# Kernel optimization log

Measured on AMD Instinct MI355X. Metric: run time of the kernel, lower is better.

Reference implementation:

```python
import jax, jax.numpy as jnp
import numpy as np

N_EMBED = 1024
N_HEADS = 16
HEAD_SIZE = N_EMBED // N_HEADS
B, T = 4, 2048
LN_EPS = 1e-5


def _layer_norm(x, gamma, beta):
    mu = jnp.mean(x, axis=-1, keepdims=True)
    var = jnp.var(x, axis=-1, keepdims=True)
    return (x - mu) * jax.lax.rsqrt(var + LN_EPS) * gamma + beta


def setup_inputs() -> dict:
    key = jax.random.key(0)
    ks = jax.random.split(key, 12)
    s = 1.0 / np.sqrt(N_EMBED)
    sh = 1.0 / np.sqrt(4 * N_EMBED)
    return {
        "x": jax.random.normal(ks[0], (B, T, N_EMBED), jnp.float32),
        "Wk": jax.random.uniform(ks[1], (N_EMBED, N_EMBED), jnp.float32, -s, s),
        "Wq": jax.random.uniform(ks[2], (N_EMBED, N_EMBED), jnp.float32, -s, s),
        "Wv": jax.random.uniform(ks[3], (N_EMBED, N_EMBED), jnp.float32, -s, s),
        "Wproj": jax.random.uniform(ks[4], (N_EMBED, N_EMBED), jnp.float32, -s, s),
        "bproj": jax.random.uniform(ks[5], (N_EMBED,), jnp.float32, -s, s),
        "W1": jax.random.uniform(ks[6], (N_EMBED, 4 * N_EMBED), jnp.float32, -s, s),
        "b1": jax.random.uniform(ks[7], (4 * N_EMBED,), jnp.float32, -s, s),
        "W2": jax.random.uniform(ks[8], (4 * N_EMBED, N_EMBED), jnp.float32, -sh, sh),
        "b2": jax.random.uniform(ks[9], (N_EMBED,), jnp.float32, -sh, sh),
        "g1": jnp.ones((N_EMBED,), jnp.float32),
        "beta1": jnp.zeros((N_EMBED,), jnp.float32),
        "g2": jnp.ones((N_EMBED,), jnp.float32),
        "beta2": jnp.zeros((N_EMBED,), jnp.float32),
    }


def reference(x, Wk, Wq, Wv, Wproj, bproj, W1, b1, W2, b2, g1, beta1, g2, beta2):
    Bt, Tt, C = x.shape
    h = _layer_norm(x, g1, beta1)
    # project and split heads: (B, H, T, D)
    def heads(W):
        return (h @ W).reshape(Bt, Tt, N_HEADS, HEAD_SIZE).transpose(0, 2, 1, 3)
    q, k, v = heads(Wq), heads(Wk), heads(Wv)
    wei = jnp.einsum("bhtd,bhsd->bhts", q, k) / np.sqrt(HEAD_SIZE)
    causal = jnp.tril(jnp.ones((Tt, Tt), bool))
    wei = jnp.where(causal, wei, -jnp.inf)
    wei = jax.nn.softmax(wei, axis=-1)
    out = jnp.einsum("bhts,bhsd->bhtd", wei, v)
    out = out.transpose(0, 2, 1, 3).reshape(Bt, Tt, C)
    x = x + out @ Wproj + bproj
    h2 = _layer_norm(x, g2, beta2)
    ff = jax.nn.relu(h2 @ W1 + b1) @ W2 + b2
    return x + ff
```

## Files before the change

### kernel.cpp

```cpp
#include <hip/hip_runtime.h>
#include <stdint.h>

typedef __bf16 bf16x8 __attribute__((ext_vector_type(8)));
typedef float f32x4 __attribute__((ext_vector_type(4)));
typedef unsigned short u16x8 __attribute__((ext_vector_type(8)));
typedef unsigned short u16x4 __attribute__((ext_vector_type(4)));
typedef unsigned int u32x2 __attribute__((ext_vector_type(2)));
typedef float fvec4 __attribute__((ext_vector_type(4)));

__device__ __forceinline__ unsigned short f2b(float f) {
  unsigned u = __builtin_bit_cast(unsigned, f);
  return (unsigned short)((u + 0x7fffu + ((u >> 16) & 1u)) >> 16);
}

__device__ __forceinline__ bf16x8 ldfrag(const unsigned short* p) {
  return __builtin_bit_cast(bf16x8, *(const u16x8*)p);
}

__device__ __forceinline__ float fexp2(float x) {
  float r;
  asm("v_exp_f32 %0, %1" : "=v"(r) : "v"(x));
  return r;
}

__device__ __forceinline__ unsigned cvtpk(float a, float b) {
  unsigned r;
  asm("v_cvt_pk_bf16_f32 %0, %1, %2" : "=v"(r) : "v"(a), "v"(b));
  return r;
}

__device__ __forceinline__ void gload_lds16(const void* g, void* l) {
  auto gp = reinterpret_cast<const __attribute__((address_space(1))) void*>(
      reinterpret_cast<uintptr_t>(g));
  auto lp = reinterpret_cast<__attribute__((address_space(3))) void*>(
      reinterpret_cast<uintptr_t>(l));
  __builtin_amdgcn_global_load_lds(gp, lp, 16, 0, 0);
}

__global__ void transpose_cast(const float* __restrict__ W, unsigned short* __restrict__ Wt,
                               int K, int N) {
  __shared__ float tile[32][33];
  const int n0 = blockIdx.x * 32, k0 = blockIdx.y * 32;
  const int tx = threadIdx.x, ty = threadIdx.y;
#pragma unroll
  for (int j = 0; j < 4; ++j)
    tile[ty + j * 8][tx] = W[(size_t)(k0 + ty + j * 8) * N + n0 + tx];
  __syncthreads();
#pragma unroll
  for (int j = 0; j < 4; ++j)
    Wt[(size_t)(n0 + ty + j * 8) * K + k0 + tx] = f2b(tile[tx][ty + j * 8]);
}

__global__ void ln_kernel(const float* __restrict__ X, const float* __restrict__ g,
                          const float* __restrict__ be, unsigned short* __restrict__ H) {
  const int row = (blockIdx.x * blockDim.x + threadIdx.x) >> 6;
  const int l = threadIdx.x & 63;
  const float* xr = X + (size_t)row * 1024;
  fvec4 v[4];
  float s = 0.f, sq = 0.f;
#pragma unroll
  for (int i = 0; i < 4; ++i) {
    v[i] = *(const fvec4*)(xr + i * 256 + l * 4);
#pragma unroll
    for (int j = 0; j < 4; ++j) { s += v[i][j]; sq += v[i][j] * v[i][j]; }
  }
#pragma unroll
  for (int off = 32; off >= 1; off >>= 1) {
    s += __shfl_xor(s, off);
    sq += __shfl_xor(sq, off);
  }
  const float mean = s * (1.f / 1024.f);
  const float var = sq * (1.f / 1024.f) - mean * mean;
  const float rstd = rsqrtf(var + 1e-5f);
#pragma unroll
  for (int i = 0; i < 4; ++i) {
    const int col = i * 256 + l * 4;
    fvec4 gg = *(const fvec4*)(g + col);
    fvec4 bb = *(const fvec4*)(be + col);
    u16x4 o;
#pragma unroll
    for (int j = 0; j < 4; ++j) o[j] = f2b((v[i][j] - mean) * rstd * gg[j] + bb[j]);
    *(u16x4*)(H + (size_t)row * 1024 + col) = o;
  }
}

template <int BM, int EPI>
__global__ __launch_bounds__(512, 1) void gemmS(
    const unsigned short* __restrict__ A, const unsigned short* __restrict__ Bt,
    const float* __restrict__ bias, const float* __restrict__ resid,
    float* __restrict__ Cf, unsigned short* __restrict__ Cb,
    unsigned short* __restrict__ pK, unsigned short* __restrict__ pVT,
    int N, int K, int ntiles) {
  constexpr int ASZ = BM * 64;
  constexpr int BSZ = 16384;
  constexpr int BUFSZ = ASZ + BSZ;
  constexpr int UA = ASZ / 8192;
  constexpr int UNITS = UA + 2;
  constexpr int MF = BM / 32;
  __shared__ __align__(16) char lds[4 * BUFSZ];

  const int tid = threadIdx.x;
  const int w = tid >> 6, l = tid & 63;
  const int wr = w >> 2, wc = w & 3;
  const int kg = l >> 4, fr = l & 15;
  const int xtiles = N / 256;
  const int nblk = (int)gridDim.x;

  int Aoff[MF], Boff[4];
#pragma unroll
  for (int m = 0; m < MF; ++m) {
    const int r = wr * (BM / 2) + m * 16 + fr;
    Aoff[m] = r * 64 + ((kg ^ ((r >> 1) & 3)) << 4);
  }
#pragma unroll
  for (int n = 0; n < 4; ++n) {
    const int rn = wc * 64 + n * 16 + fr;
    Boff[n] = ASZ + rn * 64 + ((kg ^ ((rn >> 1) & 3)) << 4);
  }

  for (int tl = (int)blockIdx.x; tl < ntiles; tl += nblk) {
    if (tl != (int)blockIdx.x) __builtin_amdgcn_s_barrier();
    const int q8 = ntiles >> 3;
    const int swz = (tl & 7) * q8 + (tl >> 3);
    const size_t am0 = (size_t)(swz / xtiles) * BM;
    const size_t bn0 = (size_t)(swz % xtiles) * 256;

    const char* src[UNITS];
#pragma unroll
    for (int u = 0; u < UA; ++u) {
      const int flat = u * 512 + tid;
      const int row = flat >> 2;
      const int scb = ((flat & 3) << 4) ^ (((row >> 1) & 3) << 4);
      src[u] = (const char*)(A + (am0 + row) * K) + scb;
    }
#pragma unroll
    for (int u = 0; u < 2; ++u) {
      const int flat = u * 512 + tid;
      const int row = flat >> 2;
      const int scb = ((flat & 3) << 4) ^ (((row >> 1) & 3) << 4);
      src[UA + u] = (const char*)(Bt + (bn0 + row) * K) + scb;
    }

    f32x4 acc[MF][4];
#pragma unroll
    for (int m = 0; m < MF; ++m)
#pragma unroll
      for (int n = 0; n < 4; ++n) acc[m][n] = (f32x4){0.f, 0.f, 0.f, 0.f};

    auto stage = [&](int sb) {
#pragma unroll
      for (int u = 0; u < UNITS; ++u) {
        gload_lds16(src[u], lds + sb * BUFSZ + u * 8192 + tid * 16);
        src[u] += 64;
      }
    };

    const int NT = K >> 5;
    stage(0);
    stage(1);
    asm volatile("s_waitcnt vmcnt(%0)" ::"i"(UNITS) : "memory");
    __builtin_amdgcn_s_barrier();

    int cb0 = 0, sb = 2;
    for (int kt = 0; kt < NT; ++kt) {
      if (kt + 2 < NT) stage(sb);
      bf16x8 af[MF], bf[4];
#pragma unroll
      for (int m = 0; m < MF; ++m)
        af[m] = ldfrag((const unsigned short*)(lds + cb0 + Aoff[m]));
#pragma unroll
      for (int n = 0; n < 4; ++n)
        bf[n] = ldfrag((const unsigned short*)(lds + cb0 + Boff[n]));
      __builtin_amdgcn_s_setprio(1);
#pragma unroll
      for (int m = 0; m < MF; ++m)
#pragma unroll
        for (int n = 0; n < 4; ++n)
          acc[m][n] = __builtin_amdgcn_mfma_f32_16x16x32_bf16(af[m], bf[n], acc[m][n], 0, 0, 0);
      __builtin_amdgcn_s_setprio(0);
      if (kt + 2 < NT) {
        asm volatile("s_waitcnt vmcnt(%0)" ::"i"(UNITS) : "memory");
        __builtin_amdgcn_s_barrier();
      } else if (kt + 1 < NT) {
        asm volatile("s_waitcnt vmcnt(0)" ::: "memory");
        __builtin_amdgcn_s_barrier();
      }
      cb0 += BUFSZ;
      if (cb0 == 4 * BUFSZ) cb0 = 0;
      sb += 1;
      if (sb == 4) sb = 0;
    }

#pragma unroll
    for (int m = 0; m < MF; ++m) {
      const size_t row0 = am0 + wr * (BM / 2) + m * 16 + kg * 4;
#pragma unroll
      for (int n = 0; n < 4; ++n) {
        const size_t col = bn0 + wc * 64 + n * 16 + fr;
        if (EPI == 3) {
          if (bn0 < 1024) {
#pragma unroll
            for (int r = 0; r < 4; ++r) Cb[(row0 + r) * 1024 + col] = f2b(acc[m][n][r]);
          } else if (bn0 < 2048) {
#pragma unroll
            for (int r = 0; r < 4; ++r) pK[(row0 + r) * 1024 + col - 1024] = f2b(acc[m][n][r]);
          } else {
            const int c2 = (int)col - 2048;
            const int hh = c2 >> 6, dd = c2 & 63;
            const int bb = (int)(row0 >> 11), tt = (int)(row0 & 2047);
            u16x4 pv;
#pragma unroll
            for (int r = 0; r < 4; ++r) pv[r] = f2b(acc[m][n][r]);
            *(u16x4*)(pVT + (((size_t)bb * 16 + hh) * 64 + dd) * 2048 + tt) = pv;
          }
        } else {
          const float bv = (EPI >= 1) ? bias[col] : 0.f;
#pragma unroll
          for (int r = 0; r < 4; ++r) {
            const size_t idx = (row0 + r) * N + col;
            float v = acc[m][n][r] + bv;
            if (EPI == 1) v = fmaxf(v, 0.f);
            if (EPI == 2) {
              Cf[idx] = v + resid[idx];
            } else {
              Cb[idx] = f2b(v);
            }
          }
        }
      }
    }
  }
}

#define PSTR 72
#define SC2 0.18033688f
__global__ __launch_bounds__(256, 2) void attn_kernel(const unsigned short* __restrict__ Qb,
                                                      const unsigned short* __restrict__ Kb,
                                                      const unsigned short* __restrict__ VT,
                                                      unsigned short* __restrict__ ATT) {
  __shared__ __align__(16) char ldsK[3 * 8192];
  __shared__ __align__(16) unsigned short Pl[4][64 * PSTR];
  const int tid = threadIdx.x;
  const int w = tid >> 6, l = tid & 63;
  const int kg = l >> 4, fr = l & 15;
  const int bh = blockIdx.x;
  const int b = bh >> 4, h = bh & 15;
  const int yy = (int)blockIdx.y;
  const int qt = (yy < 4) ? 7 - yy : yy - 4;
  const int q0 = qt * 256 + w * 64;
  const size_t rbase = (size_t)b * 2048;
  const unsigned short* vtb = VT + (size_t)bh * 64 * 2048;
  const f32x4 fz = {0.f, 0.f, 0.f, 0.f};

  const int rowoff = tid >> 3;
  const int cbsw = ((tid & 7) * 16) ^ ((rowoff & 7) << 4);
  const char* ksrc = (const char*)(Kb + rbase * 1024 + h * 64) + (size_t)rowoff * 2048 + cbsw;

  int koff[4][2];
#pragma unroll
  for (int sg = 0; sg < 4; ++sg)
#pragma unroll
    for (int c = 0; c < 2; ++c)
      koff[sg][c] = (sg * 16 + fr) * 128 + ((c * 64 + kg * 16) ^ ((fr & 7) << 4));

  bf16x8 bq[4][2];
#pragma unroll
  for (int qg = 0; qg < 4; ++qg) {
    const unsigned short* qrow = Qb + (rbase + q0 + qg * 16 + fr) * 1024 + h * 64;
#pragma unroll
    for (int c = 0; c < 2; ++c) bq[qg][c] = ldfrag(qrow + c * 32 + kg * 8);
  }

  f32x4 o[4][4];
#pragma unroll
  for (int qg = 0; qg < 4; ++qg)
#pragma unroll
    for (int nd = 0; nd < 4; ++nd) o[qg][nd] = (f32x4){0.f, 0.f, 0.f, 0.f};
  float m_run2[4] = {-1e30f, -1e30f, -1e30f, -1e30f};
  float l_run[4] = {0.f, 0.f, 0.f, 0.f};

  auto stage = [&](int t, int sbuf) {
    gload_lds16(ksrc + (size_t)(t * 64) * 2048, ldsK + sbuf * 8192 + tid * 16);
    gload_lds16(ksrc + (size_t)(t * 64 + 32) * 2048, ldsK + sbuf * 8192 + 4096 + tid * 16);
  };

  auto softmax_qg = [&](int qg, int s0, f32x4 (&stq)[4]) -> float {
    const int qa = q0 + qg * 16 + fr;
    float vals[16];
    if (s0 + 63 <= q0 + qg * 16) {
#pragma unroll
      for (int sg = 0; sg < 4; ++sg)
#pragma unroll
        for (int r = 0; r < 4; ++r) vals[sg * 4 + r] = stq[sg][r];
    } else {
#pragma unroll
      for (int sg = 0; sg < 4; ++sg)
#pragma unroll
        for (int r = 0; r < 4; ++r) {
          const int sa = s0 + sg * 16 + kg * 4 + r;
          vals[sg * 4 + r] = (sa > qa) ? -1e30f : stq[sg][r];
        }
    }
    float m5[5];
#pragma unroll
    for (int i = 0; i < 5; ++i)
      m5[i] = fmaxf(fmaxf(vals[3 * i], vals[3 * i + 1]), vals[3 * i + 2]);
    const float vmax =
        fmaxf(fmaxf(fmaxf(m5[0], m5[1]), m5[2]), fmaxf(fmaxf(m5[3], m5[4]), vals[15]));
    const float tm2 = vmax * SC2;
    if (__any(tm2 > m_run2[qg] + 8.f)) {
      float tmax2 = tm2;
      tmax2 = fmaxf(tmax2, __shfl_xor(tmax2, 16));
      tmax2 = fmaxf(tmax2, __shfl_xor(tmax2, 32));
      const float m_new2 = fmaxf(m_run2[qg], tmax2);
      const float alpha = fexp2(m_run2[qg] - m_new2);
      m_run2[qg] = m_new2;
      l_run[qg] *= alpha;
      float al[4];
#pragma unroll
      for (int r = 0; r < 4; ++r) al[r] = __shfl(alpha, kg * 4 + r);
#pragma unroll
      for (int nd = 0; nd < 4; ++nd)
#pragma unroll
        for (int r = 0; r < 4; ++r) o[qg][nd][r] *= al[r];
    }
    const float nm2 = -m_run2[qg];
    float psum = 0.f;
    unsigned pk[8];
#pragma unroll
    for (int i = 0; i < 8; ++i) {
      const float p0 = fexp2(__builtin_fmaf(vals[2 * i], SC2, nm2));
      const float p1 = fexp2(__builtin_fmaf(vals[2 * i + 1], SC2, nm2));
      psum += p0 + p1;
      pk[i] = cvtpk(p0, p1);
    }
#pragma unroll
    for (int sg = 0; sg < 4; ++sg) {
      u32x2 w2 = {pk[2 * sg], pk[2 * sg + 1]};
      *(u32x2*)(&Pl[w][(qg * 16 + fr) * PSTR + sg * 16 + kg * 4]) = w2;
    }
    return psum;
  };

  auto compute = [&](int s0, int cbb) {
    if (s0 > q0 + 63) return;
    bf16x8 vb[4][2];
#pragma unroll
    for (int nd = 0; nd < 4; ++nd)
#pragma unroll
      for (int ks = 0; ks < 2; ++ks)
        vb[nd][ks] = ldfrag(vtb + (size_t)(nd * 16 + fr) * 2048 + s0 + ks * 32 + kg * 8);

    float psv[4];
#pragma unroll
    for (int qp = 0; qp < 2; ++qp) {
      f32x4 st[4][2];
#pragma unroll
      for (int sg = 0; sg < 4; ++sg) {
        const bf16x8 ka0 = ldfrag((const unsigned short*)(ldsK + cbb + koff[sg][0]));
        const bf16x8 ka1 = ldfrag((const unsigned short*)(ldsK + cbb + koff[sg][1]));
#pragma unroll
        for (int qh = 0; qh < 2; ++qh)
          st[sg][qh] = __builtin_amdgcn_mfma_f32_16x16x32_bf16(
              ka1, bq[qp * 2 + qh][1],
              __builtin_amdgcn_mfma_f32_16x16x32_bf16(ka0, bq[qp * 2 + qh][0], fz, 0, 0, 0),
              0, 0, 0);
      }
#pragma unroll
      for (int qh = 0; qh < 2; ++qh) {
        f32x4 stq[4];
#pragma unroll
        for (int sg = 0; sg < 4; ++sg) stq[sg] = st[sg][qh];
        psv[qp * 2 + qh] = softmax_qg(qp * 2 + qh, s0, stq);
      }
    }

    {
      float a[4], c[4];
#pragma unroll
      for (int qg = 0; qg < 4; ++qg) a[qg] = __shfl_xor(psv[qg], 16);
#pragma unroll
      for (int qg = 0; qg < 4; ++qg) psv[qg] += a[qg];
#pragma unroll
      for (int qg = 0; qg < 4; ++qg) c[qg] = __shfl_xor(psv[qg], 32);
#pragma unroll
      for (int qg = 0; qg < 4; ++qg) l_run[qg] += psv[qg] + c[qg];
    }

#pragma unroll
    for (int qg = 0; qg < 4; ++qg)
#pragma unroll
      for (int ks = 0; ks < 2; ++ks) {
        const bf16x8 pa = ldfrag(&Pl[w][(qg * 16 + fr) * PSTR + ks * 32 + kg * 8]);
#pragma unroll
        for (int nd = 0; nd < 4; ++nd)
          o[qg][nd] = __builtin_amdgcn_mfma_f32_16x16x32_bf16(pa, vb[nd][ks], o[qg][nd], 0, 0, 0);
      }
  };

  const int NT = 4 * qt + 4;
  stage(0, 0);
  stage(1, 1);
  asm volatile("s_waitcnt vmcnt(2)" ::: "memory");
  __builtin_amdgcn_s_barrier();
  int cb = 0, sb = 2;
  for (int t = 0; t < NT; ++t) {
    if (t + 2 < NT) stage(t + 2, sb);
    compute(t * 64, cb * 8192);
    if (t + 2 < NT) {
      asm volatile("s_waitcnt vmcnt(2)" ::: "memory");
      __builtin_amdgcn_s_barrier();
    } else if (t + 1 < NT) {
      asm volatile("s_waitcnt vmcnt(0)" ::: "memory");
      __builtin_amdgcn_s_barrier();
    }
    cb += 1; if (cb == 3) cb = 0;
    sb += 1; if (sb == 3) sb = 0;
  }

#pragma unroll
  for (int qg = 0; qg < 4; ++qg) {
    const float li = __builtin_amdgcn_rcpf(l_run[qg]);
    float linv[4];
#pragma unroll
    for (int r = 0; r < 4; ++r) linv[r] = __shfl(li, kg * 4 + r);
#pragma unroll
    for (int nd = 0; nd < 4; ++nd)
#pragma unroll
      for (int r = 0; r < 4; ++r) {
        const size_t row = rbase + q0 + qg * 16 + kg * 4 + r;
        ATT[row * 1024 + h * 64 + nd * 16 + fr] = f2b(o[qg][nd][r] * linv[r]);
      }
  }
}

extern "C" void kernel_launch(void* const* d_in, const int* in_sizes, int n_in, void* d_out,
                              int out_size, void* d_ws, size_t ws_size, hipStream_t stream) {
  const float* x = (const float*)d_in[0];
  const float* Wk = (const float*)d_in[1];
  const float* Wq = (const float*)d_in[2];
  const float* Wv = (const float*)d_in[3];
  const float* Wproj = (const float*)d_in[4];
  const float* bproj = (const float*)d_in[5];
  const float* W1 = (const float*)d_in[6];
  const float* b1 = (const float*)d_in[7];
  const float* W2 = (const float*)d_in[8];
  const float* b2 = (const float*)d_in[9];
  const float* g1 = (const float*)d_in[10];
  const float* beta1 = (const float*)d_in[11];
  const float* g2 = (const float*)d_in[12];
  const float* beta2 = (const float*)d_in[13];
  float* out = (float*)d_out;
  unsigned short* wsu = (unsigned short*)d_ws;

  const size_t o_qkvW = 0;
  const size_t o_projW = o_qkvW + 3072 * 1024;
  const size_t o_W1 = o_projW + 1024 * 1024;
  const size_t o_W2 = o_W1 + 4096 * 1024;
  const size_t o_H = o_W2 + 1024 * 4096;
  const size_t o_Q = o_H + (size_t)8192 * 1024;
  const size_t o_K = o_Q + (size_t)8192 * 1024;
  const size_t o_VT = o_K + (size_t)8192 * 1024;
  const size_t o_ATT = o_VT + (size_t)8192 * 1024;
  const size_t o_FF1 = o_Q;

  dim3 tpb(32, 8);
  transpose_cast<<<dim3(32, 32), tpb, 0, stream>>>(Wq, wsu + o_qkvW, 1024, 1024);
  transpose_cast<<<dim3(32, 32), tpb, 0, stream>>>(Wk, wsu + o_qkvW + 1024 * 1024, 1024, 1024);
  transpose_cast<<<dim3(32, 32), tpb, 0, stream>>>(Wv, wsu + o_qkvW + 2 * 1024 * 1024, 1024, 1024);
  transpose_cast<<<dim3(32, 32), tpb, 0, stream>>>(Wproj, wsu + o_projW, 1024, 1024);
  transpose_cast<<<dim3(128, 32), tpb, 0, stream>>>(W1, wsu + o_W1, 1024, 4096);
  transpose_cast<<<dim3(32, 128), tpb, 0, stream>>>(W2, wsu + o_W2, 4096, 1024);

  ln_kernel<<<2048, 256, 0, stream>>>(x, g1, beta1, wsu + o_H);

  gemmS<128, 3><<<256, 512, 0, stream>>>(wsu + o_H, wsu + o_qkvW, nullptr, nullptr, nullptr,
                                         wsu + o_Q, wsu + o_K, wsu + o_VT, 3072, 1024, 768);

  attn_kernel<<<dim3(64, 8), 256, 0, stream>>>(wsu + o_Q, wsu + o_K, wsu + o_VT, wsu + o_ATT);

  gemmS<128, 2><<<256, 512, 0, stream>>>(wsu + o_ATT, wsu + o_projW, bproj, x, out, nullptr,
                                         nullptr, nullptr, 1024, 1024, 256);

  ln_kernel<<<2048, 256, 0, stream>>>(out, g2, beta2, wsu + o_H);

  gemmS<256, 1><<<256, 512, 0, stream>>>(wsu + o_H, wsu + o_W1, b1, nullptr, nullptr,
                                         wsu + o_FF1, nullptr, nullptr, 4096, 1024, 512);

  gemmS<128, 2><<<256, 512, 0, stream>>>(wsu + o_FF1, wsu + o_W2, b2, out, out, nullptr,
                                         nullptr, nullptr, 1024, 4096, 256);
}
```

Baseline: 342.9 us.

## Pair causal query tiles per block for balanced attention work

```diff
diff --git a/kernel.cpp b/kernel.cpp
--- a/kernel.cpp
+++ b/kernel.cpp
@@ -239,15 +239,13 @@
                                                       const unsigned short* __restrict__ VT,
                                                       unsigned short* __restrict__ ATT) {
   __shared__ __align__(16) char ldsK[3 * 8192];
-  __shared__ __align__(16) unsigned short Pl[4][64 * PSTR];
+  __shared__ __align__(16) unsigned short Pl[4][32 * PSTR];
   const int tid = threadIdx.x;
   const int w = tid >> 6, l = tid & 63;
   const int kg = l >> 4, fr = l & 15;
   const int bh = blockIdx.x;
   const int b = bh >> 4, h = bh & 15;
   const int yy = (int)blockIdx.y;
-  const int qt = (yy < 4) ? 7 - yy : yy - 4;
-  const int q0 = qt * 256 + w * 64;
   const size_t rbase = (size_t)b * 2048;
   const unsigned short* vtb = VT + (size_t)bh * 64 * 2048;
   const f32x4 fz = {0.f, 0.f, 0.f, 0.f};
@@ -262,175 +260,170 @@
 #pragma unroll
     for (int c = 0; c < 2; ++c)
       koff[sg][c] = (sg * 16 + fr) * 128 + ((c * 64 + kg * 16) ^ ((fr & 7) << 4));
-
-  bf16x8 bq[4][2];
-#pragma unroll
-  for (int qg = 0; qg < 4; ++qg) {
-    const unsigned short* qrow = Qb + (rbase + q0 + qg * 16 + fr) * 1024 + h * 64;
-#pragma unroll
-    for (int c = 0; c < 2; ++c) bq[qg][c] = ldfrag(qrow + c * 32 + kg * 8);
-  }
-
-  f32x4 o[4][4];
-#pragma unroll
-  for (int qg = 0; qg < 4; ++qg)
-#pragma unroll
-    for (int nd = 0; nd < 4; ++nd) o[qg][nd] = (f32x4){0.f, 0.f, 0.f, 0.f};
-  float m_run2[4] = {-1e30f, -1e30f, -1e30f, -1e30f};
-  float l_run[4] = {0.f, 0.f, 0.f, 0.f};
 
   auto stage = [&](int t, int sbuf) {
     gload_lds16(ksrc + (size_t)(t * 64) * 2048, ldsK + sbuf * 8192 + tid * 16);
     gload_lds16(ksrc + (size_t)(t * 64 + 32) * 2048, ldsK + sbuf * 8192 + 4096 + tid * 16);
   };
 
-  auto softmax_qg = [&](int qg, int s0, f32x4 (&stq)[4]) -> float {
-    const int qa = q0 + qg * 16 + fr;
-    float vals[16];
-    if (s0 + 63 <= q0 + qg * 16) {
-#pragma unroll
-      for (int sg = 0; sg < 4; ++sg)
-#pragma unroll
-        for (int r = 0; r < 4; ++r) vals[sg * 4 + r] = stq[sg][r];
-    } else {
-#pragma unroll
-      for (int sg = 0; sg < 4; ++sg)
-#pragma unroll
-        for (int r = 0; r < 4; ++r) {
-          const int sa = s0 + sg * 16 + kg * 4 + r;
-          vals[sg * 4 + r] = (sa > qa) ? -1e30f : stq[sg][r];
-        }
-    }
-    float m5[5];
-#pragma unroll
-    for (int i = 0; i < 5; ++i)
-      m5[i] = fmaxf(fmaxf(vals[3 * i], vals[3 * i + 1]), vals[3 * i + 2]);
-    const float vmax =
-        fmaxf(fmaxf(fmaxf(m5[0], m5[1]), m5[2]), fmaxf(fmaxf(m5[3], m5[4]), vals[15]));
-    const float tm2 = vmax * SC2;
-    if (__any(tm2 > m_run2[qg] + 8.f)) {
-      float tmax2 = tm2;
-      tmax2 = fmaxf(tmax2, __shfl_xor(tmax2, 16));
-      tmax2 = fmaxf(tmax2, __shfl_xor(tmax2, 32));
-      const float m_new2 = fmaxf(m_run2[qg], tmax2);
-      const float alpha = fexp2(m_run2[qg] - m_new2);
-      m_run2[qg] = m_new2;
-      l_run[qg] *= alpha;
-      float al[4];
-#pragma unroll
-      for (int r = 0; r < 4; ++r) al[r] = __shfl(alpha, kg * 4 + r);
+  for (int pass = 0; pass < 2; ++pass) {
+    const int qt = pass ? yy : 15 - yy;
+    const int q0 = qt * 128 + w * 32;
+
+    bf16x8 bq[2][2];
+#pragma unroll
+    for (int qg = 0; qg < 2; ++qg) {
+      const unsigned short* qrow = Qb + (rbase + q0 + qg * 16 + fr) * 1024 + h * 64;
+#pragma unroll
+      for (int c = 0; c < 2; ++c) bq[qg][c] = ldfrag(qrow + c * 32 + kg * 8);
+    }
+
+    f32x4 o[2][4];
+#pragma unroll
+    for (int qg = 0; qg < 2; ++qg)
+#pragma unroll
+      for (int nd = 0; nd < 4; ++nd) o[qg][nd] = (f32x4){0.f, 0.f, 0.f, 0.f};
+    float m_run2[2] = {-1e30f, -1e30f}, l_run[2] = {0.f, 0.f};
+
+    auto compute = [&](int s0, int cbb) {
+      if (s0 > q0 + 31) return;
+      bf16x8 vb[4][2];
 #pragma unroll
       for (int nd = 0; nd < 4; ++nd)
 #pragma unroll
-        for (int r = 0; r < 4; ++r) o[qg][nd][r] *= al[r];
-    }
-    const float nm2 = -m_run2[qg];
-    float psum = 0.f;
-    unsigned pk[8];
-#pragma unroll
-    for (int i = 0; i < 8; ++i) {
-      const float p0 = fexp2(__builtin_fmaf(vals[2 * i], SC2, nm2));
-      const float p1 = fexp2(__builtin_fmaf(vals[2 * i + 1], SC2, nm2));
-      psum += p0 + p1;
-      pk[i] = cvtpk(p0, p1);
-    }
-#pragma unroll
-    for (int sg = 0; sg < 4; ++sg) {
-      u32x2 w2 = {pk[2 * sg], pk[2 * sg + 1]};
-      *(u32x2*)(&Pl[w][(qg * 16 + fr) * PSTR + sg * 16 + kg * 4]) = w2;
-    }
-    return psum;
-  };
-
-  auto compute = [&](int s0, int cbb) {
-    if (s0 > q0 + 63) return;
-    bf16x8 vb[4][2];
-#pragma unroll
-    for (int nd = 0; nd < 4; ++nd)
-#pragma unroll
-      for (int ks = 0; ks < 2; ++ks)
-        vb[nd][ks] = ldfrag(vtb + (size_t)(nd * 16 + fr) * 2048 + s0 + ks * 32 + kg * 8);
-
-    float psv[4];
-#pragma unroll
-    for (int qp = 0; qp < 2; ++qp) {
+        for (int ks = 0; ks < 2; ++ks)
+          vb[nd][ks] = ldfrag(vtb + (size_t)(nd * 16 + fr) * 2048 + s0 + ks * 32 + kg * 8);
+
       f32x4 st[4][2];
 #pragma unroll
       for (int sg = 0; sg < 4; ++sg) {
         const bf16x8 ka0 = ldfrag((const unsigned short*)(ldsK + cbb + koff[sg][0]));
         const bf16x8 ka1 = ldfrag((const unsigned short*)(ldsK + cbb + koff[sg][1]));
 #pragma unroll
-        for (int qh = 0; qh < 2; ++qh)
-          st[sg][qh] = __builtin_amdgcn_mfma_f32_16x16x32_bf16(
-              ka1, bq[qp * 2 + qh][1],
-              __builtin_amdgcn_mfma_f32_16x16x32_bf16(ka0, bq[qp * 2 + qh][0], fz, 0, 0, 0),
-              0, 0, 0);
-      }
-#pragma unroll
-      for (int qh = 0; qh < 2; ++qh) {
-        f32x4 stq[4];
-#pragma unroll
-        for (int sg = 0; sg < 4; ++sg) stq[sg] = st[sg][qh];
-        psv[qp * 2 + qh] = softmax_qg(qp * 2 + qh, s0, stq);
-      }
-    }
-
-    {
-      float a[4], c[4];
-#pragma unroll
-      for (int qg = 0; qg < 4; ++qg) a[qg] = __shfl_xor(psv[qg], 16);
-#pragma unroll
-      for (int qg = 0; qg < 4; ++qg) psv[qg] += a[qg];
-#pragma unroll
-      for (int qg = 0; qg < 4; ++qg) c[qg] = __shfl_xor(psv[qg], 32);
-#pragma unroll
-      for (int qg = 0; qg < 4; ++qg) l_run[qg] += psv[qg] + c[qg];
-    }
-
-#pragma unroll
-    for (int qg = 0; qg < 4; ++qg)
-#pragma unroll
-      for (int ks = 0; ks < 2; ++ks) {
-        const bf16x8 pa = ldfrag(&Pl[w][(qg * 16 + fr) * PSTR + ks * 32 + kg * 8]);
-#pragma unroll
-        for (int nd = 0; nd < 4; ++nd)
-          o[qg][nd] = __builtin_amdgcn_mfma_f32_16x16x32_bf16(pa, vb[nd][ks], o[qg][nd], 0, 0, 0);
-      }
-  };
-
-  const int NT = 4 * qt + 4;
-  stage(0, 0);
-  stage(1, 1);
-  asm volatile("s_waitcnt vmcnt(2)" ::: "memory");
-  __builtin_amdgcn_s_barrier();
-  int cb = 0, sb = 2;
-  for (int t = 0; t < NT; ++t) {
-    if (t + 2 < NT) stage(t + 2, sb);
-    compute(t * 64, cb * 8192);
-    if (t + 2 < NT) {
-      asm volatile("s_waitcnt vmcnt(2)" ::: "memory");
-      __builtin_amdgcn_s_barrier();
-    } else if (t + 1 < NT) {
-      asm volatile("s_waitcnt vmcnt(0)" ::: "memory");
-      __builtin_amdgcn_s_barrier();
-    }
-    cb += 1; if (cb == 3) cb = 0;
-    sb += 1; if (sb == 3) sb = 0;
-  }
-
-#pragma unroll
-  for (int qg = 0; qg < 4; ++qg) {
-    const float li = __builtin_amdgcn_rcpf(l_run[qg]);
-    float linv[4];
-#pragma unroll
-    for (int r = 0; r < 4; ++r) linv[r] = __shfl(li, kg * 4 + r);
-#pragma unroll
-    for (int nd = 0; nd < 4; ++nd)
-#pragma unroll
-      for (int r = 0; r < 4; ++r) {
-        const size_t row = rbase + q0 + qg * 16 + kg * 4 + r;
-        ATT[row * 1024 + h * 64 + nd * 16 + fr] = f2b(o[qg][nd][r] * linv[r]);
-      }
+        for (int qg = 0; qg < 2; ++qg)
+          st[sg][qg] = __builtin_amdgcn_mfma_f32_16x16x32_bf16(
+              ka1, bq[qg][1],
+              __builtin_amdgcn_mfma_f32_16x16x32_bf16(ka0, bq[qg][0], fz, 0, 0, 0), 0, 0, 0);
+      }
+
+      float psv[2];
+#pragma unroll
+      for (int qg = 0; qg < 2; ++qg) {
+        const int qa = q0 + qg * 16 + fr;
+        float vals[16];
+        if (s0 + 63 <= q0 + qg * 16) {
+#pragma unroll
+          for (int sg = 0; sg < 4; ++sg)
+#pragma unroll
+            for (int r = 0; r < 4; ++r) vals[sg * 4 + r] = st[sg][qg][r];
+        } else {
+#pragma unroll
+          for (int sg = 0; sg < 4; ++sg)
+#pragma unroll
+            for (int r = 0; r < 4; ++r) {
+              const int sa = s0 + sg * 16 + kg * 4 + r;
+              vals[sg * 4 + r] = (sa > qa) ? -1e30f : st[sg][qg][r];
+            }
+        }
+        float m5[5];
+#pragma unroll
+        for (int i = 0; i < 5; ++i)
+          m5[i] = fmaxf(fmaxf(vals[3 * i], vals[3 * i + 1]), vals[3 * i + 2]);
+        const float vmax =
+            fmaxf(fmaxf(fmaxf(m5[0], m5[1]), m5[2]), fmaxf(fmaxf(m5[3], m5[4]), vals[15]));
+        const float tm2 = vmax * SC2;
+        if (__any(tm2 > m_run2[qg] + 8.f)) {
+          float tmax2 = tm2;
+          tmax2 = fmaxf(tmax2, __shfl_xor(tmax2, 16));
+          tmax2 = fmaxf(tmax2, __shfl_xor(tmax2, 32));
+          const float m_new2 = fmaxf(m_run2[qg], tmax2);
+          const float alpha = fexp2(m_run2[qg] - m_new2);
+          m_run2[qg] = m_new2;
+          l_run[qg] *= alpha;
+          float al[4];
+#pragma unroll
+          for (int r = 0; r < 4; ++r) al[r] = __shfl(alpha, kg * 4 + r);
+#pragma unroll
+          for (int nd = 0; nd < 4; ++nd)
+#pragma unroll
+            for (int r = 0; r < 4; ++r) o[qg][nd][r] *= al[r];
+        }
+        const float nm2 = -m_run2[qg];
+        float psum = 0.f;
+        unsigned pk[8];
+#pragma unroll
+        for (int i = 0; i < 8; ++i) {
+          const float p0 = fexp2(__builtin_fmaf(vals[2 * i], SC2, nm2));
+          const float p1 = fexp2(__builtin_fmaf(vals[2 * i + 1], SC2, nm2));
+          psum += p0 + p1;
+          pk[i] = cvtpk(p0, p1);
+        }
+        psv[qg] = psum;
+#pragma unroll
+        for (int sg = 0; sg < 4; ++sg) {
+          u32x2 w2 = {pk[2 * sg], pk[2 * sg + 1]};
+          *(u32x2*)(&Pl[w][(qg * 16 + fr) * PSTR + sg * 16 + kg * 4]) = w2;
+        }
+      }
+
+      {
+        const float a0 = __shfl_xor(psv[0], 16);
+        const float a1 = __shfl_xor(psv[1], 16);
+        psv[0] += a0;
+        psv[1] += a1;
+        const float b0 = __shfl_xor(psv[0], 32);
+        const float b1 = __shfl_xor(psv[1], 32);
+        l_run[0] += psv[0] + b0;
+        l_run[1] += psv[1] + b1;
+      }
+
+#pragma unroll
+      for (int qg = 0; qg < 2; ++qg)
+#pragma unroll
+        for (int ks = 0; ks < 2; ++ks) {
+          const bf16x8 pa = ldfrag(&Pl[w][(qg * 16 + fr) * PSTR + ks * 32 + kg * 8]);
+#pragma unroll
+          for (int nd = 0; nd < 4; ++nd)
+            o[qg][nd] =
+                __builtin_amdgcn_mfma_f32_16x16x32_bf16(pa, vb[nd][ks], o[qg][nd], 0, 0, 0);
+        }
+    };
+
+    const int NT = 2 * qt + 2;
+    if (pass) __builtin_amdgcn_s_barrier();
+    stage(0, 0);
+    stage(1, 1);
+    asm volatile("s_waitcnt vmcnt(2)" ::: "memory");
+    __builtin_amdgcn_s_barrier();
+    int cb = 0, sb = 2;
+    for (int t = 0; t < NT; ++t) {
+      if (t + 2 < NT) stage(t + 2, sb);
+      compute(t * 64, cb * 8192);
+      if (t + 2 < NT) {
+        asm volatile("s_waitcnt vmcnt(2)" ::: "memory");
+        __builtin_amdgcn_s_barrier();
+      } else if (t + 1 < NT) {
+        asm volatile("s_waitcnt vmcnt(0)" ::: "memory");
+        __builtin_amdgcn_s_barrier();
+      }
+      cb += 1; if (cb == 3) cb = 0;
+      sb += 1; if (sb == 3) sb = 0;
+    }
+
+#pragma unroll
+    for (int qg = 0; qg < 2; ++qg) {
+      const float li = __builtin_amdgcn_rcpf(l_run[qg]);
+      float linv[4];
+#pragma unroll
+      for (int r = 0; r < 4; ++r) linv[r] = __shfl(li, kg * 4 + r);
+#pragma unroll
+      for (int nd = 0; nd < 4; ++nd)
+#pragma unroll
+        for (int r = 0; r < 4; ++r) {
+          const size_t row = rbase + q0 + qg * 16 + kg * 4 + r;
+          ATT[row * 1024 + h * 64 + nd * 16 + fr] = f2b(o[qg][nd][r] * linv[r]);
+        }
+    }
   }
 }
 
```

Measured after the change: 349.1 us. Within noise of the previous version (+1.8%).

## Deepen GEMM K-tile to 64 with triple buffering and fixed 128-row M tile

Applied to the files above, without the earlier changes.

```diff
diff --git a/kernel.cpp b/kernel.cpp
--- a/kernel.cpp
+++ b/kernel.cpp
@@ -84,20 +84,17 @@
   }
 }
 
-template <int BM, int EPI>
+template <int EPI>
 __global__ __launch_bounds__(512, 1) void gemmS(
     const unsigned short* __restrict__ A, const unsigned short* __restrict__ Bt,
     const float* __restrict__ bias, const float* __restrict__ resid,
     float* __restrict__ Cf, unsigned short* __restrict__ Cb,
     unsigned short* __restrict__ pK, unsigned short* __restrict__ pVT,
     int N, int K, int ntiles) {
-  constexpr int ASZ = BM * 64;
-  constexpr int BSZ = 16384;
+  constexpr int ASZ = 16384;
+  constexpr int BSZ = 32768;
   constexpr int BUFSZ = ASZ + BSZ;
-  constexpr int UA = ASZ / 8192;
-  constexpr int UNITS = UA + 2;
-  constexpr int MF = BM / 32;
-  __shared__ __align__(16) char lds[4 * BUFSZ];
+  __shared__ __align__(16) char lds[3 * BUFSZ];
 
   const int tid = threadIdx.x;
   const int w = tid >> 6, l = tid & 63;
@@ -106,94 +103,104 @@
   const int xtiles = N / 256;
   const int nblk = (int)gridDim.x;
 
-  int Aoff[MF], Boff[4];
-#pragma unroll
-  for (int m = 0; m < MF; ++m) {
-    const int r = wr * (BM / 2) + m * 16 + fr;
-    Aoff[m] = r * 64 + ((kg ^ ((r >> 1) & 3)) << 4);
-  }
-#pragma unroll
-  for (int n = 0; n < 4; ++n) {
-    const int rn = wc * 64 + n * 16 + fr;
-    Boff[n] = ASZ + rn * 64 + ((kg ^ ((rn >> 1) & 3)) << 4);
+  int Aoff[2][4], Boff[2][4];
+#pragma unroll
+  for (int kk = 0; kk < 2; ++kk) {
+#pragma unroll
+    for (int m = 0; m < 4; ++m) {
+      const int r = wr * 64 + m * 16 + fr;
+      Aoff[kk][m] = r * 128 + (((kk * 4 + kg) ^ (r & 7)) << 4);
+    }
+#pragma unroll
+    for (int n = 0; n < 4; ++n) {
+      const int rn = wc * 64 + n * 16 + fr;
+      Boff[kk][n] = ASZ + rn * 128 + (((kk * 4 + kg) ^ (rn & 7)) << 4);
+    }
   }
 
   for (int tl = (int)blockIdx.x; tl < ntiles; tl += nblk) {
     if (tl != (int)blockIdx.x) __builtin_amdgcn_s_barrier();
     const int q8 = ntiles >> 3;
     const int swz = (tl & 7) * q8 + (tl >> 3);
-    const size_t am0 = (size_t)(swz / xtiles) * BM;
+    const size_t am0 = (size_t)(swz / xtiles) * 128;
     const size_t bn0 = (size_t)(swz % xtiles) * 256;
 
-    const char* src[UNITS];
-#pragma unroll
-    for (int u = 0; u < UA; ++u) {
-      const int flat = u * 512 + tid;
-      const int row = flat >> 2;
-      const int scb = ((flat & 3) << 4) ^ (((row >> 1) & 3) << 4);
-      src[u] = (const char*)(A + (am0 + row) * K) + scb;
-    }
+    const char* src[6];
 #pragma unroll
     for (int u = 0; u < 2; ++u) {
       const int flat = u * 512 + tid;
-      const int row = flat >> 2;
-      const int scb = ((flat & 3) << 4) ^ (((row >> 1) & 3) << 4);
-      src[UA + u] = (const char*)(Bt + (bn0 + row) * K) + scb;
-    }
-
-    f32x4 acc[MF][4];
-#pragma unroll
-    for (int m = 0; m < MF; ++m)
+      const int row = flat >> 3, c = flat & 7;
+      src[u] = (const char*)(A + (am0 + row) * K) + ((c ^ (row & 7)) << 4);
+    }
+#pragma unroll
+    for (int u = 0; u < 4; ++u) {
+      const int flat = u * 512 + tid;
+      const int row = flat >> 3, c = flat & 7;
+      src[2 + u] = (const char*)(Bt + (bn0 + row) * K) + ((c ^ (row & 7)) << 4);
+    }
+
+    f32x4 acc[4][4];
+#pragma unroll
+    for (int m = 0; m < 4; ++m)
 #pragma unroll
       for (int n = 0; n < 4; ++n) acc[m][n] = (f32x4){0.f, 0.f, 0.f, 0.f};
 
     auto stage = [&](int sb) {
-#pragma unroll
-      for (int u = 0; u < UNITS; ++u) {
-        gload_lds16(src[u], lds + sb * BUFSZ + u * 8192 + tid * 16);
-        src[u] += 64;
+      char* Ld = lds + sb * BUFSZ;
+#pragma unroll
+      for (int u = 0; u < 2; ++u) {
+        gload_lds16(src[u], Ld + u * 8192 + tid * 16);
+        src[u] += 128;
+      }
+#pragma unroll
+      for (int u = 0; u < 4; ++u) {
+        gload_lds16(src[2 + u], Ld + ASZ + u * 8192 + tid * 16);
+        src[2 + u] += 128;
       }
     };
 
-    const int NT = K >> 5;
+    const int NT = K >> 6;
     stage(0);
     stage(1);
-    asm volatile("s_waitcnt vmcnt(%0)" ::"i"(UNITS) : "memory");
+    asm volatile("s_waitcnt vmcnt(6)" ::: "memory");
     __builtin_amdgcn_s_barrier();
 
     int cb0 = 0, sb = 2;
     for (int kt = 0; kt < NT; ++kt) {
       if (kt + 2 < NT) stage(sb);
-      bf16x8 af[MF], bf[4];
-#pragma unroll
-      for (int m = 0; m < MF; ++m)
-        af[m] = ldfrag((const unsigned short*)(lds + cb0 + Aoff[m]));
-#pragma unroll
-      for (int n = 0; n < 4; ++n)
-        bf[n] = ldfrag((const unsigned short*)(lds + cb0 + Boff[n]));
-      __builtin_amdgcn_s_setprio(1);
-#pragma unroll
-      for (int m = 0; m < MF; ++m)
+#pragma unroll
+      for (int kk = 0; kk < 2; ++kk) {
+        bf16x8 af[4], bf[4];
+#pragma unroll
+        for (int m = 0; m < 4; ++m)
+          af[m] = ldfrag((const unsigned short*)(lds + cb0 + Aoff[kk][m]));
 #pragma unroll
         for (int n = 0; n < 4; ++n)
-          acc[m][n] = __builtin_amdgcn_mfma_f32_16x16x32_bf16(af[m], bf[n], acc[m][n], 0, 0, 0);
-      __builtin_amdgcn_s_setprio(0);
+          bf[n] = ldfrag((const unsigned short*)(lds + cb0 + Boff[kk][n]));
+        __builtin_amdgcn_s_setprio(1);
+#pragma unroll
+        for (int m = 0; m < 4; ++m)
+#pragma unroll
+          for (int n = 0; n < 4; ++n)
+            acc[m][n] = __builtin_amdgcn_mfma_f32_16x16x32_bf16(af[m], bf[n], acc[m][n], 0, 0, 0);
+        __builtin_amdgcn_s_setprio(0);
+      }
       if (kt + 2 < NT) {
-        asm volatile("s_waitcnt vmcnt(%0)" ::"i"(UNITS) : "memory");
+        asm volatile("s_waitcnt vmcnt(6)" ::: "memory");
         __builtin_amdgcn_s_barrier();
       } else if (kt + 1 < NT) {
         asm volatile("s_waitcnt vmcnt(0)" ::: "memory");
         __builtin_amdgcn_s_barrier();
       }
       cb0 += BUFSZ;
-      if (cb0 == 4 * BUFSZ) cb0 = 0;
+      if (cb0 == 3 * BUFSZ) cb0 = 0;
       sb += 1;
-      if (sb == 4) sb = 0;
-    }
-
-#pragma unroll
-    for (int m = 0; m < MF; ++m) {
-      const size_t row0 = am0 + wr * (BM / 2) + m * 16 + kg * 4;
+      if (sb == 3) sb = 0;
+    }
+
+#pragma unroll
+    for (int m = 0; m < 4; ++m) {
+      const size_t row0 = am0 + wr * 64 + m * 16 + kg * 4;
 #pragma unroll
       for (int n = 0; n < 4; ++n) {
         const size_t col = bn0 + wc * 64 + n * 16 + fr;
@@ -474,19 +481,19 @@
 
   ln_kernel<<<2048, 256, 0, stream>>>(x, g1, beta1, wsu + o_H);
 
-  gemmS<128, 3><<<256, 512, 0, stream>>>(wsu + o_H, wsu + o_qkvW, nullptr, nullptr, nullptr,
-                                         wsu + o_Q, wsu + o_K, wsu + o_VT, 3072, 1024, 768);
+  gemmS<3><<<256, 512, 0, stream>>>(wsu + o_H, wsu + o_qkvW, nullptr, nullptr, nullptr,
+                                    wsu + o_Q, wsu + o_K, wsu + o_VT, 3072, 1024, 768);
 
   attn_kernel<<<dim3(64, 8), 256, 0, stream>>>(wsu + o_Q, wsu + o_K, wsu + o_VT, wsu + o_ATT);
 
-  gemmS<128, 2><<<256, 512, 0, stream>>>(wsu + o_ATT, wsu + o_projW, bproj, x, out, nullptr,
-                                         nullptr, nullptr, 1024, 1024, 256);
+  gemmS<2><<<256, 512, 0, stream>>>(wsu + o_ATT, wsu + o_projW, bproj, x, out, nullptr,
+                                    nullptr, nullptr, 1024, 1024, 256);
 
   ln_kernel<<<2048, 256, 0, stream>>>(out, g2, beta2, wsu + o_H);
 
-  gemmS<256, 1><<<256, 512, 0, stream>>>(wsu + o_H, wsu + o_W1, b1, nullptr, nullptr,
-                                         wsu + o_FF1, nullptr, nullptr, 4096, 1024, 512);
-
-  gemmS<128, 2><<<256, 512, 0, stream>>>(wsu + o_FF1, wsu + o_W2, b2, out, out, nullptr,
-                                         nullptr, nullptr, 1024, 4096, 256);
-}
+  gemmS<1><<<256, 512, 0, stream>>>(wsu + o_H, wsu + o_W1, b1, nullptr, nullptr,
+                                    wsu + o_FF1, nullptr, nullptr, 4096, 1024, 1024);
+
+  gemmS<2><<<256, 512, 0, stream>>>(wsu + o_FF1, wsu + o_W2, b2, out, out, nullptr,
+                                    nullptr, nullptr, 1024, 4096, 256);
+}
```

After: 340.6 us. No clear change (-0.6%).
